# Kernel tuning notes

Hardware: AMD Instinct MI355X
Metric: run time of the kernel (lower is better)

Reference implementation:

```python
import jax, jax.numpy as jnp
import numpy as np

B = 65536
SHARED_DIMS = [(937, 512), (512, 512), (512, 256), (256, 256), (256, 256), (256, 256), (256, 256)]
HEAD_DIMS_V = [(256, 128), (128, 64), (64, 1)]
HEAD_DIMS_A = [(256, 128), (128, 64), (64, 4)]


def _init_params(key, dims, prefix):
    out = {}
    for i, (fi, fo) in enumerate(dims):
        key, k1, k2 = jax.random.split(key, 3)
        s = 1.0 / np.sqrt(fi)
        out[f"{prefix}w{i+1}"] = jax.random.uniform(k1, (fi, fo), jnp.float32, -s, s)
        out[f"{prefix}b{i+1}"] = jax.random.uniform(k2, (fo,), jnp.float32, -s, s)
    return out, key


def setup_inputs() -> dict:
    key = jax.random.key(0)
    k1, k2, k3, key = jax.random.split(key, 4)
    inp = {
        "x": jax.random.normal(k1, (B, 937), jnp.float32),
        "suicides": jax.random.randint(k2, (B, 4), 0, 2).astype(bool),
        "invalid_actions": jax.random.randint(k3, (B,), 0, 4),
    }
    p, key = _init_params(key, SHARED_DIMS, "s")
    inp.update(p)
    p, key = _init_params(key, HEAD_DIMS_V, "v")
    inp.update(p)
    p, key = _init_params(key, HEAD_DIMS_A, "a")
    inp.update(p)
    return inp


def _mlp_relu_all(h, ws_bs):
    # Linear+ReLU after every layer (shared trunk ends with ReLU)
    for w, b in ws_bs:
        h = jax.nn.relu(h @ w + b)
    return h


def _head(h, ws_bs):
    # ReLU after all but last layer
    for w, b in ws_bs[:-1]:
        h = jax.nn.relu(h @ w + b)
    w, b = ws_bs[-1]
    return h @ w + b


def reference(x, suicides, invalid_actions,
              sw1, sb1, sw2, sb2, sw3, sb3, sw4, sb4, sw5, sb5, sw6, sb6, sw7, sb7,
              vw1, vb1, vw2, vb2, vw3, vb3,
              aw1, ab1, aw2, ab2, aw3, ab3):
    h = _mlp_relu_all(x, [(sw1, sb1), (sw2, sb2), (sw3, sb3), (sw4, sb4), (sw5, sb5), (sw6, sb6), (sw7, sb7)])
    values = _head(h, [(vw1, vb1), (vw2, vb2), (vw3, vb3)])          # [B,1]
    adv = _head(h, [(aw1, ab1), (aw2, ab2), (aw3, ab3)])             # [B,4]

    all_s = jnp.all(suicides, axis=1)                                 # [B]
    onehot_inv = jnp.arange(4)[None, :] == invalid_actions[:, None]   # [B,4]
    # if all suicides: only the invalid action is masked, denom=3
    # else: suicide actions masked, denom = #non-suicide actions
    mask = jnp.where(all_s[:, None], onehot_inv, suicides)            # [B,4]
    denom = jnp.where(all_s, 3.0, jnp.sum(~suicides, axis=1).astype(jnp.float32))
    means = jnp.sum(jnp.where(mask, 0.0, adv), axis=1) / denom        # [B]
    adv_masked = jnp.where(mask, -jnp.inf, adv)
    return values + (adv_masked - means[:, None])                     # [B,4]
```

## Files before the change

kernel.cpp:

```cpp
#include <hip/hip_runtime.h>
#include <hip/hip_bf16.h>

typedef __attribute__((ext_vector_type(8))) short short8;
typedef __attribute__((ext_vector_type(4))) float f32x4;

#define B_ROWS 65536

__device__ inline unsigned short f2bf(float v) {
    __hip_bfloat16 h = __float2bfloat16(v);
    unsigned short u;
    __builtin_memcpy(&u, &h, 2);
    return u;
}

__device__ inline float bf2f(unsigned short u) {
    union { unsigned int i; float f; } cv;
    cv.i = ((unsigned int)u) << 16;
    return cv.f;
}

__global__ __launch_bounds__(256) void convert_x_kernel(const float* __restrict__ x,
                                                        __hip_bfloat16* __restrict__ xb) {
    __shared__ __attribute__((aligned(16))) unsigned short ls[960];
    const int r = blockIdx.x;
    const int t = threadIdx.x;
    const float* xr = x + (size_t)r * 937;
#pragma unroll
    for (int p = 0; p < 4; ++p) {
        int c = t + p * 256;
        if (c < 937) ls[c] = f2bf(xr[c]);
        else if (c < 960) ls[c] = 0;
    }
    __syncthreads();
    if (t < 120)
        *(short8*)(xb + (size_t)r * 960 + t * 8) = *(const short8*)&ls[t * 8];
}

struct WDesc { const float* src; __hip_bfloat16* dst; int N, K, Npad, Kpad; };
struct WDescs { WDesc d[7]; };

__global__ void prep_weights_kernel(WDescs descs) {
    WDesc w = descs.d[blockIdx.y];
    int kg_count = w.Kpad >> 3;
    int per = w.Npad * kg_count;
    for (int i = blockIdx.x * blockDim.x + threadIdx.x; i < per; i += gridDim.x * blockDim.x) {
        int n = i % w.Npad;
        int kg = i / w.Npad;
        int k0 = kg << 3;
        short8 r;
#pragma unroll
        for (int j = 0; j < 8; ++j) {
            int k = k0 + j;
            float v = (n < w.N && k < w.K) ? w.src[(size_t)k * w.N + n] : 0.0f;
            r[j] = (short)f2bf(v);
        }
        *(short8*)((char*)w.dst + ((size_t)n * w.Kpad + (size_t)k0) * 2) = r;
    }
}

struct TailArgs {
    const float *vw1, *vb1, *aw1, *ab1, *vw2, *vb2, *aw2, *ab2;
    const float *b4, *b5, *b6, *b7;
    __hip_bfloat16* Wtail;
    float* Bs;
};

__global__ void prep_tail_kernel(TailArgs a) {
    int g = blockIdx.x * 256 + threadIdx.x;
    int half = g >> 16;
    int j = g & 65535;
    int n = j >> 8, k = j & 255;
    float v;
    if (half == 0) {
        v = (n < 128) ? a.vw1[(size_t)k * 128 + n] : a.aw1[(size_t)k * 128 + (n - 128)];
    } else {
        if (n < 64 && k < 128)                 v = a.vw2[(size_t)k * 64 + n];
        else if (n >= 64 && n < 128 && k >= 128) v = a.aw2[(size_t)(k - 128) * 64 + (n - 64)];
        else                                   v = 0.0f;
    }
    a.Wtail[(size_t)(4 + half) * 65536 + j] = __float2bfloat16(v);

    if (g < 1536) {
        int l = g >> 8, nn = g & 255;
        float bv;
        if (l == 0) bv = a.b4[nn];
        else if (l == 1) bv = a.b5[nn];
        else if (l == 2) bv = a.b6[nn];
        else if (l == 3) bv = a.b7[nn];
        else if (l == 4) bv = (nn < 128) ? a.vb1[nn] : a.ab1[nn - 128];
        else             bv = (nn < 64) ? a.vb2[nn] : (nn < 128 ? a.ab2[nn - 64] : 0.0f);
        a.Bs[g] = bv;
    }
}

#define BM 128
#define BN 128
#define BK 64

__global__ __launch_bounds__(256) void gemm_bias_relu(
    const __hip_bfloat16* __restrict__ A,
    const __hip_bfloat16* __restrict__ Bt,
    const float* __restrict__ bias,
    __hip_bfloat16* __restrict__ C,
    int K, int N, int relu)
{
    __shared__ __attribute__((aligned(16))) __hip_bfloat16 sA[BM][BK];
    __shared__ __attribute__((aligned(16))) __hip_bfloat16 sB[BN][BK];

    const int t = threadIdx.x;
    const int wid = t >> 6;
    const int lane = t & 63;
    const int brow = blockIdx.x * BM;
    const int bcol = blockIdx.y * BN;
    const int wr = wid >> 1, wc = wid & 1;

    f32x4 acc[4][4] = {};

    const __hip_bfloat16* ga = A + (size_t)(brow + (t >> 3)) * K + (t & 7) * 8;
    const __hip_bfloat16* gb = Bt + (size_t)(bcol + (t >> 3)) * K + (t & 7) * 8;

    for (int k0 = 0; k0 < K; k0 += BK) {
#pragma unroll
        for (int it = 0; it < 4; ++it) {
            __builtin_amdgcn_global_load_lds(
                (const __attribute__((address_space(1))) void*)(ga + (size_t)it * 32 * K + k0),
                (__attribute__((address_space(3))) void*)((char*)&sA[0][0] + it * 4096 + wid * 1024),
                16, 0, 0);
            __builtin_amdgcn_global_load_lds(
                (const __attribute__((address_space(1))) void*)(gb + (size_t)it * 32 * K + k0),
                (__attribute__((address_space(3))) void*)((char*)&sB[0][0] + it * 4096 + wid * 1024),
                16, 0, 0);
        }
        __syncthreads();
#pragma unroll
        for (int kk = 0; kk < 2; ++kk) {
            short8 af[4], bfr[4];
#pragma unroll
            for (int m = 0; m < 4; ++m)
                af[m] = *(const short8*)&sA[wr * 64 + m * 16 + (lane & 15)][kk * 32 + (lane >> 4) * 8];
#pragma unroll
            for (int n = 0; n < 4; ++n)
                bfr[n] = *(const short8*)&sB[wc * 64 + n * 16 + (lane & 15)][kk * 32 + (lane >> 4) * 8];
#pragma unroll
            for (int m = 0; m < 4; ++m)
#pragma unroll
                for (int n = 0; n < 4; ++n)
                    acc[m][n] = __builtin_amdgcn_mfma_f32_16x16x32_bf16(af[m], bfr[n], acc[m][n], 0, 0, 0);
        }
        __syncthreads();
    }

    float biasv[4];
#pragma unroll
    for (int n = 0; n < 4; ++n) {
        int col = bcol + wc * 64 + n * 16 + (lane & 15);
        biasv[n] = (col < N) ? bias[col] : 0.0f;
    }
#pragma unroll
    for (int m = 0; m < 4; ++m) {
        int row = brow + wr * 64 + m * 16 + ((lane >> 4) << 2);
#pragma unroll
        for (int n = 0; n < 4; ++n) {
            int col = bcol + wc * 64 + n * 16 + (lane & 15);
            if (col < N) {
#pragma unroll
                for (int r = 0; r < 4; ++r) {
                    float v = acc[m][n][r] + biasv[n];
                    if (relu) v = fmaxf(v, 0.0f);
                    C[(size_t)(row + r) * N + col] = __float2bfloat16(v);
                }
            }
        }
    }
}


__device__ __forceinline__ char* swzp(char* base, int row, int byte_in_row) {
    return base + row * 512 + (byte_in_row ^ ((row & 7) << 4));
}

__global__ __launch_bounds__(256, 2) void fused_tail(
    const __hip_bfloat16* __restrict__ h3,
    const __hip_bfloat16* __restrict__ Wtail,
    const float* __restrict__ Bs,
    const float* __restrict__ vw3, const float* __restrict__ vb3,
    const float* __restrict__ aw3, const float* __restrict__ ab3,
    const int* __restrict__ suicides, const int* __restrict__ invalid,
    float* __restrict__ out)
{
    __shared__ __attribute__((aligned(16))) unsigned char sAct[128 * 512];
    __shared__ float svw[64];
    __shared__ float saw[256];

    const int t = threadIdx.x;
    const int wid = t >> 6;
    const int lane = t & 63;
    const int brow = blockIdx.x * 128;
    const int wnbase = wid * 64;

    if (t < 64) svw[t] = vw3[t];
    saw[t] = aw3[t];

    {
        const __hip_bfloat16* src = h3 + (size_t)brow * 256;
        int r = t >> 1, c0 = (t & 1) * 128;
#pragma unroll
        for (int j = 0; j < 16; ++j) {
            short8 v = *(const short8*)(src + (size_t)r * 256 + c0 + j * 8);
            *(short8*)swzp((char*)sAct, r, (c0 + j * 8) * 2) = v;
        }
    }
    __syncthreads();

    for (int layer = 0; layer < 6; ++layer) {
        const __hip_bfloat16* W = Wtail + (size_t)layer * 65536;
        const float* bias = Bs + layer * 256;

        f32x4 acc[8][4] = {};
#pragma unroll
        for (int kk = 0; kk < 8; ++kk) {
            short8 bfrag[4];
#pragma unroll
            for (int n = 0; n < 4; ++n)
                bfrag[n] = *(const short8*)(W + (size_t)(wnbase + n * 16 + (lane & 15)) * 256
                                            + kk * 32 + (lane >> 4) * 8);
            short8 afrag[8];
#pragma unroll
            for (int m = 0; m < 8; ++m) {
                int r = m * 16 + (lane & 15);
                afrag[m] = *(const short8*)swzp((char*)sAct, r, (kk * 32 + (lane >> 4) * 8) * 2);
            }
#pragma unroll
            for (int m = 0; m < 8; ++m)
#pragma unroll
                for (int n = 0; n < 4; ++n)
                    acc[m][n] = __builtin_amdgcn_mfma_f32_16x16x32_bf16(afrag[m], bfrag[n], acc[m][n], 0, 0, 0);
        }
        __syncthreads();

        float bv[4];
#pragma unroll
        for (int n = 0; n < 4; ++n) bv[n] = bias[wnbase + n * 16 + (lane & 15)];
#pragma unroll
        for (int m = 0; m < 8; ++m) {
#pragma unroll
            for (int n = 0; n < 4; ++n) {
                int col = wnbase + n * 16 + (lane & 15);
#pragma unroll
                for (int r4 = 0; r4 < 4; ++r4) {
                    int row = m * 16 + ((lane >> 4) << 2) + r4;
                    float v = fmaxf(acc[m][n][r4] + bv[n], 0.0f);
                    *(unsigned short*)swzp((char*)sAct, row, col * 2) = f2bf(v);
                }
            }
        }
        __syncthreads();
    }

    if (t < 128) {
        int grow = brow + t;
        float vsum = vb3[0];
        float a0 = ab3[0], a1 = ab3[1], a2v = ab3[2], a3v = ab3[3];
#pragma unroll
        for (int k = 0; k < 64; ++k) {
            float hv = bf2f(*(unsigned short*)swzp((char*)sAct, t, k * 2));
            float ha = bf2f(*(unsigned short*)swzp((char*)sAct, t, (64 + k) * 2));
            vsum += hv * svw[k];
            a0 += ha * saw[k * 4 + 0];
            a1 += ha * saw[k * 4 + 1];
            a2v += ha * saw[k * 4 + 2];
            a3v += ha * saw[k * 4 + 3];
        }
        float adv[4] = { a0, a1, a2v, a3v };

        int4 sv = *(const int4*)(suicides + (size_t)grow * 4);
        int s0 = sv.x != 0, s1 = sv.y != 0, s2 = sv.z != 0, s3 = sv.w != 0;
        int all_s = s0 & s1 & s2 & s3;
        int inv = invalid[grow];

        int sarr[4] = { s0, s1, s2, s3 };
        bool mask[4];
#pragma unroll
        for (int jj = 0; jj < 4; ++jj)
            mask[jj] = all_s ? (jj == inv) : (sarr[jj] != 0);

        float denom = all_s ? 3.0f : (float)(4 - (s0 + s1 + s2 + s3));
        float sum = 0.0f;
#pragma unroll
        for (int jj = 0; jj < 4; ++jj) if (!mask[jj]) sum += adv[jj];
        float mean = sum / denom;

        float ninf = -1.0e30f;
        float4 o;
        o.x = mask[0] ? ninf : vsum + adv[0] - mean;
        o.y = mask[1] ? ninf : vsum + adv[1] - mean;
        o.z = mask[2] ? ninf : vsum + adv[2] - mean;
        o.w = mask[3] ? ninf : vsum + adv[3] - mean;
        *(float4*)(out + (size_t)grow * 4) = o;
    }
}

extern "C" void kernel_launch(void* const* d_in, const int* in_sizes, int n_in,
                              void* d_out, int out_size, void* d_ws, size_t ws_size,
                              hipStream_t stream) {
    const float* x = (const float*)d_in[0];
    const int* suicides = (const int*)d_in[1];
    const int* invalid = (const int*)d_in[2];

    char* ws = (char*)d_ws;
    size_t off = 0;
    auto alloc = [&](size_t bytes) { char* p = ws + off; off += (bytes + 255) & ~(size_t)255; return p; };

    __hip_bfloat16* wT1 = (__hip_bfloat16*)alloc((size_t)512 * 960 * 2);
    __hip_bfloat16* wT2 = (__hip_bfloat16*)alloc((size_t)512 * 512 * 2);
    __hip_bfloat16* wT3 = (__hip_bfloat16*)alloc((size_t)256 * 512 * 2);
    __hip_bfloat16* Wtail = (__hip_bfloat16*)alloc((size_t)6 * 65536 * 2);
    float* Bs = (float*)alloc((size_t)6 * 256 * 4);

    __hip_bfloat16* actA = (__hip_bfloat16*)alloc((size_t)B_ROWS * 960 * 2);
    __hip_bfloat16* actB = (__hip_bfloat16*)alloc((size_t)B_ROWS * 512 * 2);

    WDescs descs;
    descs.d[0] = { (const float*)d_in[3],  wT1,              512, 937, 512, 960 };
    descs.d[1] = { (const float*)d_in[5],  wT2,              512, 512, 512, 512 };
    descs.d[2] = { (const float*)d_in[7],  wT3,              256, 512, 256, 512 };
    descs.d[3] = { (const float*)d_in[9],  Wtail + 0 * 65536, 256, 256, 256, 256 };
    descs.d[4] = { (const float*)d_in[11], Wtail + 1 * 65536, 256, 256, 256, 256 };
    descs.d[5] = { (const float*)d_in[13], Wtail + 2 * 65536, 256, 256, 256, 256 };
    descs.d[6] = { (const float*)d_in[15], Wtail + 3 * 65536, 256, 256, 256, 256 };
    prep_weights_kernel<<<dim3(240, 7), 256, 0, stream>>>(descs);

    TailArgs ta;
    ta.vw1 = (const float*)d_in[17]; ta.vb1 = (const float*)d_in[18];
    ta.vw2 = (const float*)d_in[19]; ta.vb2 = (const float*)d_in[20];
    ta.aw1 = (const float*)d_in[23]; ta.ab1 = (const float*)d_in[24];
    ta.aw2 = (const float*)d_in[25]; ta.ab2 = (const float*)d_in[26];
    ta.b4 = (const float*)d_in[10]; ta.b5 = (const float*)d_in[12];
    ta.b6 = (const float*)d_in[14]; ta.b7 = (const float*)d_in[16];
    ta.Wtail = Wtail; ta.Bs = Bs;
    prep_tail_kernel<<<512, 256, 0, stream>>>(ta);

    convert_x_kernel<<<B_ROWS, 256, 0, stream>>>(x, actA);

    auto gemm = [&](const __hip_bfloat16* A, const __hip_bfloat16* Bt, const float* bias,
                    __hip_bfloat16* C, int K, int N, int Npad, int relu) {
        dim3 grid(B_ROWS / BM, Npad / BN);
        gemm_bias_relu<<<grid, 256, 0, stream>>>(A, Bt, bias, C, K, N, relu);
    };

    gemm(actA, wT1, (const float*)d_in[4], actB, 960, 512, 512, 1);
    gemm(actB, wT2, (const float*)d_in[6], actA, 512, 512, 512, 1);
    gemm(actA, wT3, (const float*)d_in[8], actB, 512, 256, 256, 1);

    fused_tail<<<B_ROWS / 128, 256, 0, stream>>>(
        actB, Wtail, Bs,
        (const float*)d_in[21], (const float*)d_in[22],
        (const float*)d_in[27], (const float*)d_in[28],
        suicides, invalid, (float*)d_out);

    (void)in_sizes; (void)n_in; (void)out_size; (void)ws_size;
}
```

Baseline: 825.1 us.

## Split fused tail across 8 waves and parallelize head dot products

The fused tail kernel goes from 4 waves to 8 waves per 128-row block. Each wave now computes a 64x64 output tile instead of 128x64, which halves the accumulator registers per wave and lets more waves hide latency. The final head projection is spread over four threads per row using vectorized LDS reads and a shuffle reduction, where before a single thread handled each row serially. The cost is more redundant global weight-fragment loads, since each weight tile is now fetched by two waves, and launch_bounds(512,4) may squeeze registers.

```diff
diff --git a/kernel.cpp b/kernel.cpp
--- a/kernel.cpp
+++ b/kernel.cpp
@@ -179,7 +179,7 @@
     return base + row * 512 + (byte_in_row ^ ((row & 7) << 4));
 }
 
-__global__ __launch_bounds__(256, 2) void fused_tail(
+__global__ __launch_bounds__(512, 4) void fused_tail(
     const __hip_bfloat16* __restrict__ h3,
     const __hip_bfloat16* __restrict__ Wtail,
     const float* __restrict__ Bs,
@@ -196,16 +196,19 @@
     const int wid = t >> 6;
     const int lane = t & 63;
     const int brow = blockIdx.x * 128;
-    const int wnbase = wid * 64;
+    const int wr = wid >> 2;
+    const int wc = wid & 3;
+    const int mrbase = wr * 64;
+    const int wnbase = wc * 64;
 
     if (t < 64) svw[t] = vw3[t];
-    saw[t] = aw3[t];
+    if (t < 256) saw[t] = aw3[t];
 
     {
         const __hip_bfloat16* src = h3 + (size_t)brow * 256;
-        int r = t >> 1, c0 = (t & 1) * 128;
-#pragma unroll
-        for (int j = 0; j < 16; ++j) {
+        int r = t >> 2, c0 = (t & 3) * 64;
+#pragma unroll
+        for (int j = 0; j < 8; ++j) {
             short8 v = *(const short8*)(src + (size_t)r * 256 + c0 + j * 8);
             *(short8*)swzp((char*)sAct, r, (c0 + j * 8) * 2) = v;
         }
@@ -216,7 +219,7 @@
         const __hip_bfloat16* W = Wtail + (size_t)layer * 65536;
         const float* bias = Bs + layer * 256;
 
-        f32x4 acc[8][4] = {};
+        f32x4 acc[4][4] = {};
 #pragma unroll
         for (int kk = 0; kk < 8; ++kk) {
             short8 bfrag[4];
@@ -224,14 +227,14 @@
             for (int n = 0; n < 4; ++n)
                 bfrag[n] = *(const short8*)(W + (size_t)(wnbase + n * 16 + (lane & 15)) * 256
                                             + kk * 32 + (lane >> 4) * 8);
-            short8 afrag[8];
-#pragma unroll
-            for (int m = 0; m < 8; ++m) {
-                int r = m * 16 + (lane & 15);
+            short8 afrag[4];
+#pragma unroll
+            for (int m = 0; m < 4; ++m) {
+                int r = mrbase + m * 16 + (lane & 15);
                 afrag[m] = *(const short8*)swzp((char*)sAct, r, (kk * 32 + (lane >> 4) * 8) * 2);
             }
 #pragma unroll
-            for (int m = 0; m < 8; ++m)
+            for (int m = 0; m < 4; ++m)
 #pragma unroll
                 for (int n = 0; n < 4; ++n)
                     acc[m][n] = __builtin_amdgcn_mfma_f32_16x16x32_bf16(afrag[m], bfrag[n], acc[m][n], 0, 0, 0);
@@ -242,13 +245,13 @@
 #pragma unroll
         for (int n = 0; n < 4; ++n) bv[n] = bias[wnbase + n * 16 + (lane & 15)];
 #pragma unroll
-        for (int m = 0; m < 8; ++m) {
+        for (int m = 0; m < 4; ++m) {
 #pragma unroll
             for (int n = 0; n < 4; ++n) {
                 int col = wnbase + n * 16 + (lane & 15);
 #pragma unroll
                 for (int r4 = 0; r4 < 4; ++r4) {
-                    int row = m * 16 + ((lane >> 4) << 2) + r4;
+                    int row = mrbase + m * 16 + ((lane >> 4) << 2) + r4;
                     float v = fmaxf(acc[m][n][r4] + bv[n], 0.0f);
                     *(unsigned short*)swzp((char*)sAct, row, col * 2) = f2bf(v);
                 }
@@ -257,46 +260,65 @@
         __syncthreads();
     }
 
-    if (t < 128) {
-        int grow = brow + t;
-        float vsum = vb3[0];
-        float a0 = ab3[0], a1 = ab3[1], a2v = ab3[2], a3v = ab3[3];
-#pragma unroll
-        for (int k = 0; k < 64; ++k) {
-            float hv = bf2f(*(unsigned short*)swzp((char*)sAct, t, k * 2));
-            float ha = bf2f(*(unsigned short*)swzp((char*)sAct, t, (64 + k) * 2));
-            vsum += hv * svw[k];
-            a0 += ha * saw[k * 4 + 0];
-            a1 += ha * saw[k * 4 + 1];
-            a2v += ha * saw[k * 4 + 2];
-            a3v += ha * saw[k * 4 + 3];
-        }
-        float adv[4] = { a0, a1, a2v, a3v };
-
-        int4 sv = *(const int4*)(suicides + (size_t)grow * 4);
-        int s0 = sv.x != 0, s1 = sv.y != 0, s2 = sv.z != 0, s3 = sv.w != 0;
-        int all_s = s0 & s1 & s2 & s3;
-        int inv = invalid[grow];
-
-        int sarr[4] = { s0, s1, s2, s3 };
-        bool mask[4];
-#pragma unroll
-        for (int jj = 0; jj < 4; ++jj)
-            mask[jj] = all_s ? (jj == inv) : (sarr[jj] != 0);
-
-        float denom = all_s ? 3.0f : (float)(4 - (s0 + s1 + s2 + s3));
-        float sum = 0.0f;
-#pragma unroll
-        for (int jj = 0; jj < 4; ++jj) if (!mask[jj]) sum += adv[jj];
-        float mean = sum / denom;
-
-        float ninf = -1.0e30f;
-        float4 o;
-        o.x = mask[0] ? ninf : vsum + adv[0] - mean;
-        o.y = mask[1] ? ninf : vsum + adv[1] - mean;
-        o.z = mask[2] ? ninf : vsum + adv[2] - mean;
-        o.w = mask[3] ? ninf : vsum + adv[3] - mean;
-        *(float4*)(out + (size_t)grow * 4) = o;
+    {
+        int row = t >> 2;
+        int part = t & 3;
+        int k0 = part * 16;
+
+        float vsum = 0.0f;
+        float a0 = 0.0f, a1 = 0.0f, a2v = 0.0f, a3v = 0.0f;
+#pragma unroll
+        for (int h = 0; h < 2; ++h) {
+            short8 hv8 = *(const short8*)swzp((char*)sAct, row, (k0 + h * 8) * 2);
+            short8 ha8 = *(const short8*)swzp((char*)sAct, row, (64 + k0 + h * 8) * 2);
+#pragma unroll
+            for (int j = 0; j < 8; ++j) {
+                int k = k0 + h * 8 + j;
+                float hv = bf2f((unsigned short)hv8[j]);
+                float ha = bf2f((unsigned short)ha8[j]);
+                vsum += hv * svw[k];
+                a0 += ha * saw[k * 4 + 0];
+                a1 += ha * saw[k * 4 + 1];
+                a2v += ha * saw[k * 4 + 2];
+                a3v += ha * saw[k * 4 + 3];
+            }
+        }
+        vsum += __shfl_xor(vsum, 1); vsum += __shfl_xor(vsum, 2);
+        a0 += __shfl_xor(a0, 1);   a0 += __shfl_xor(a0, 2);
+        a1 += __shfl_xor(a1, 1);   a1 += __shfl_xor(a1, 2);
+        a2v += __shfl_xor(a2v, 1); a2v += __shfl_xor(a2v, 2);
+        a3v += __shfl_xor(a3v, 1); a3v += __shfl_xor(a3v, 2);
+
+        if (part == 0) {
+            int grow = brow + row;
+            float value = vsum + vb3[0];
+            float adv[4] = { a0 + ab3[0], a1 + ab3[1], a2v + ab3[2], a3v + ab3[3] };
+
+            int4 sv = *(const int4*)(suicides + (size_t)grow * 4);
+            int s0 = sv.x != 0, s1 = sv.y != 0, s2 = sv.z != 0, s3 = sv.w != 0;
+            int all_s = s0 & s1 & s2 & s3;
+            int inv = invalid[grow];
+
+            int sarr[4] = { s0, s1, s2, s3 };
+            bool mask[4];
+#pragma unroll
+            for (int jj = 0; jj < 4; ++jj)
+                mask[jj] = all_s ? (jj == inv) : (sarr[jj] != 0);
+
+            float denom = all_s ? 3.0f : (float)(4 - (s0 + s1 + s2 + s3));
+            float sum = 0.0f;
+#pragma unroll
+            for (int jj = 0; jj < 4; ++jj) if (!mask[jj]) sum += adv[jj];
+            float mean = sum / denom;
+
+            float ninf = -1.0e30f;
+            float4 o;
+            o.x = mask[0] ? ninf : value + adv[0] - mean;
+            o.y = mask[1] ? ninf : value + adv[1] - mean;
+            o.z = mask[2] ? ninf : value + adv[2] - mean;
+            o.w = mask[3] ? ninf : value + adv[3] - mean;
+            *(float4*)(out + (size_t)grow * 4) = o;
+        }
     }
 }
 
@@ -352,7 +374,7 @@
     gemm(actB, wT2, (const float*)d_in[6], actA, 512, 512, 512, 1);
     gemm(actA, wT3, (const float*)d_in[8], actB, 512, 256, 256, 1);
 
-    fused_tail<<<B_ROWS / 128, 256, 0, stream>>>(
+    fused_tail<<<B_ROWS / 128, 512, 0, stream>>>(
         actB, Wtail, Bs,
         (const float*)d_in[21], (const float*)d_in[22],
         (const float*)d_in[27], (const float*)d_in[28],
```

Result: no change. 838.8 us (+1.7%).
